# Kernel tuning notes

Hardware: AMD Instinct MI355X
Metric: run time of the kernel (lower is better)

The kernel has to match this reference:

```python
import jax, jax.numpy as jnp
import numpy as np

D_MODEL = 1024
NUM_HEADS = 16
HEAD_DIM = D_MODEL // NUM_HEADS
THETA = 10000.0
B, S = 1, 2048


def setup_inputs() -> dict:
    key = jax.random.key(0)
    ks = jax.random.split(key, 7)
    sc = 0.02
    return {
        "query": jax.random.normal(ks[0], (B, S, D_MODEL), jnp.float32),
        "key": jax.random.normal(ks[1], (B, S, D_MODEL), jnp.float32),
        "value": jax.random.normal(ks[2], (B, S, D_MODEL), jnp.float32),
        "qkv_w": jax.random.normal(ks[3], (3 * D_MODEL, D_MODEL), jnp.float32) * sc,
        "qkv_b": jax.random.normal(ks[4], (3 * D_MODEL,), jnp.float32) * sc,
        "out_w": jax.random.normal(ks[5], (D_MODEL, D_MODEL), jnp.float32) * sc,
        "out_b": jax.random.normal(ks[6], (D_MODEL,), jnp.float32) * sc,
    }


def _rope_cos_sin(seq_len, head_dim, dtype):
    # freqs_for='lang': inv_freq = theta^(-2i/d), i = 0..d/2-1
    inv_freq = 1.0 / (THETA ** (jnp.arange(0, head_dim, 2, dtype=jnp.float32) / head_dim))
    t = jnp.arange(seq_len, dtype=jnp.float32)
    freqs = jnp.outer(t, inv_freq)                      # [S, d/2]
    emb = jnp.concatenate([freqs, freqs], axis=-1)      # [S, d] (non-interleaved)
    return jnp.cos(emb).astype(dtype), jnp.sin(emb).astype(dtype)


def _rotate_half(x):
    half = x.shape[-1] // 2
    return jnp.concatenate([-x[..., half:], x[..., :half]], axis=-1)


def reference(query, key, value, qkv_w, qkv_b, out_w, out_b):
    # NOTE: module computes q,k,v all from `query` (key/value args unused).
    b, s, d = query.shape
    qkv = query @ qkv_w.T + qkv_b                       # [B,S,3D]
    qkv = qkv.reshape(b, s, 3, NUM_HEADS, HEAD_DIM)
    qkv = jnp.transpose(qkv, (2, 0, 3, 1, 4))           # [3,B,H,S,hd]
    q, k, v = qkv[0], qkv[1], qkv[2]

    cos, sin = _rope_cos_sin(s, HEAD_DIM, query.dtype)  # [S,hd]
    q = q * cos + _rotate_half(q) * sin
    k = k * cos + _rotate_half(k) * sin

    scale = 1.0 / np.sqrt(HEAD_DIM)
    scores = jnp.einsum('bhqd,bhkd->bhqk', q, k) * scale
    attn = jax.nn.softmax(scores, axis=-1)
    ctx = jnp.einsum('bhqk,bhkd->bhqd', attn, v)        # [B,H,S,hd]
    ctx = jnp.transpose(ctx, (0, 2, 1, 3)).reshape(b, s, d)
    return ctx @ out_w.T + out_b
```

## Files before the change

kernel.cpp:

```cpp
#include <hip/hip_runtime.h>
#include <math.h>
#include <stdint.h>

#define SEQ 2048
#define DM  1024
#define NH  16
#define HD  64
#define TRI 3072

typedef _Float16 half8 __attribute__((ext_vector_type(8)));
typedef float f32x4 __attribute__((ext_vector_type(4)));

#define GLOAD_LDS16(g, l)                                       \
  __builtin_amdgcn_global_load_lds(                             \
      (__attribute__((address_space(1))) void*)(g),             \
      (__attribute__((address_space(3))) void*)(l), 16, 0, 0)

__global__ __launch_bounds__(256)
void cvt3(const float* __restrict__ s1, const float* __restrict__ s2,
          const float* __restrict__ s3, _Float16* __restrict__ d1,
          _Float16* __restrict__ d2, _Float16* __restrict__ d3,
          float2* __restrict__ tab, int n1, int n2) {
  int b = blockIdx.x;
  if (b >= 6144) {
    int i = (b - 6144) * 256 + threadIdx.x;
    int s = i >> 5, d = i & 31;
    float inv = exp2f((float)d * -0.4152410118609203f);
    float ang = (float)s * inv;
    float sn, cs;
    sincosf(ang, &sn, &cs);
    tab[i] = make_float2(cs, sn);
    return;
  }
  int i = (b * 256 + threadIdx.x) * 4;
  const float* s; _Float16* d;
  if (i < n1)            { s = s1; d = d1; }
  else if (i < n1 + n2)  { s = s2; d = d2; i -= n1; }
  else                   { s = s3; d = d3; i -= n1 + n2; }
  float4 v = *(const float4*)(s + i);
  union { _Float16 h[4]; uint2 u; } pk;
  pk.h[0] = (_Float16)v.x; pk.h[1] = (_Float16)v.y;
  pk.h[2] = (_Float16)v.z; pk.h[3] = (_Float16)v.w;
  *(uint2*)(d + i) = pk.u;
}

template<int ROPE, typename OutT>
__global__ __launch_bounds__(256)
void gemm_dbuf(const _Float16* __restrict__ A, const _Float16* __restrict__ B,
               const float* __restrict__ bias, const float2* __restrict__ tab,
               OutT* __restrict__ C, int M, int N, int K) {
  __shared__ _Float16 As[2][64 * 32];
  __shared__ _Float16 Bs[2][128 * 32];

  const int t = threadIdx.x, lane = t & 63, wv = t >> 6;
  const int l15 = lane & 15, l4 = lane >> 4;
  const int wr = wv >> 1, wc = wv & 1;
  const int bm = blockIdx.y * 64, bn = blockIdx.x * 128;

  auto stage = [&](int buf, int k0) {
    {
      int c = t;
      GLOAD_LDS16(A + (size_t)(bm + (c >> 2)) * K + k0 + (c & 3) * 8,
                  (char*)&As[buf][wv * 512]);
    }
    #pragma unroll
    for (int i = 0; i < 2; ++i) {
      int c = t + i * 256;
      GLOAD_LDS16(B + (size_t)(bn + (c >> 2)) * K + k0 + (c & 3) * 8,
                  (char*)&Bs[buf][(i * 256 + wv * 64) * 8]);
    }
  };

  f32x4 acc[2][4] = {};
  stage(0, 0);
  __syncthreads();

  const int nk = K / 32;
  for (int s = 0; s < nk; ++s) {
    int cur = s & 1;
    if (s + 1 < nk) stage(cur ^ 1, (s + 1) * 32);
    half8 af[2], bf[4];
    #pragma unroll
    for (int mf = 0; mf < 2; ++mf)
      af[mf] = *(const half8*)&As[cur][(wr * 32 + mf * 16 + l15) * 32 + l4 * 8];
    #pragma unroll
    for (int nf = 0; nf < 4; ++nf)
      bf[nf] = *(const half8*)&Bs[cur][(wc * 64 + nf * 16 + l15) * 32 + l4 * 8];
    __builtin_amdgcn_s_setprio(1);
    #pragma unroll
    for (int mf = 0; mf < 2; ++mf)
      #pragma unroll
      for (int nf = 0; nf < 4; ++nf)
        acc[mf][nf] = __builtin_amdgcn_mfma_f32_16x16x32_f16(
            af[mf], bf[nf], acc[mf][nf], 0, 0, 0);
    __builtin_amdgcn_s_setprio(0);
    __syncthreads();
  }

  const int sec = ROPE ? (bn >> 10) : 2;
  float bv[4];
  #pragma unroll
  for (int nf = 0; nf < 4; ++nf) bv[nf] = bias[bn + wc * 64 + nf * 16 + l15];
  #pragma unroll
  for (int mf = 0; mf < 2; ++mf)
    #pragma unroll
    for (int r = 0; r < 4; ++r) {
      int row = bm + wr * 32 + mf * 16 + l4 * 4 + r;
      float v0 = acc[mf][0][r] + bv[0];
      float v1 = acc[mf][1][r] + bv[1];
      float v2 = acc[mf][2][r] + bv[2];
      float v3 = acc[mf][3][r] + bv[3];
      if (ROPE && sec < 2) {
        float2 cs0 = tab[row * 32 + l15];
        float2 cs1 = tab[row * 32 + 16 + l15];
        float a0 = v0 * cs0.x - v2 * cs0.y;
        float a2 = v2 * cs0.x + v0 * cs0.y;
        float a1 = v1 * cs1.x - v3 * cs1.y;
        float a3 = v3 * cs1.x + v1 * cs1.y;
        if (sec == 0) { a0 *= 0.125f; a1 *= 0.125f; a2 *= 0.125f; a3 *= 0.125f; }
        v0 = a0; v1 = a1; v2 = a2; v3 = a3;
      }
      OutT* cr = C + (size_t)row * N + bn + wc * 64 + l15;
      cr[0]  = (OutT)v0; cr[16] = (OutT)v1;
      cr[32] = (OutT)v2; cr[48] = (OutT)v3;
    }
}

__global__ __launch_bounds__(256)
void attn_f16(const _Float16* __restrict__ qkv, _Float16* __restrict__ ctx) {
  __shared__ _Float16 Kl[2][64 * 64];
  __shared__ _Float16 Vt[2][64 * 64];
  __shared__ _Float16 Pl[4][16 * 72];

  const int t = threadIdx.x, lane = t & 63, wv = t >> 6;
  const int l15 = lane & 15, l4 = lane >> 4;
  const int h = blockIdx.y, q0 = blockIdx.x * 64;

  const _Float16* Qb = qkv + h * HD;
  const _Float16* Kb = qkv + DM + h * HD;
  const _Float16* Vb = qkv + 2 * DM + h * HD;

  half8 qf[2];
  {
    const _Float16* qrow = Qb + (size_t)(q0 + wv * 16 + l15) * TRI;
    qf[0] = *(const half8*)(qrow + l4 * 8);
    qf[1] = *(const half8*)(qrow + 32 + l4 * 8);
  }

  uint4 vreg[2];

  auto issueK = [&](int buf, int kt) {
    #pragma unroll
    for (int i = 0; i < 2; ++i) {
      int c = t + i * 256, r = c >> 3, p = c & 7;
      GLOAD_LDS16(Kb + (size_t)(kt + r) * TRI + ((p ^ (r & 7)) * 8),
                  (char*)&Kl[buf][(i * 256 + wv * 64) * 8]);
    }
  };
  auto issueV = [&](int kt) {
    #pragma unroll
    for (int i = 0; i < 2; ++i)
      vreg[i] = *(const uint4*)(Vb + (size_t)(kt + lane) * TRI + (wv + i * 4) * 8);
  };
  auto writeV = [&](int buf) {
    const int m = lane & 3, k0 = lane & 60;
    #pragma unroll
    for (int i = 0; i < 2; ++i) {
      uint32_t u0 = vreg[i].x, u1 = vreg[i].y, u2 = vreg[i].z, u3 = vreg[i].w;
      uint32_t s0 = __shfl_xor(u1, 1), s1 = __shfl_xor(u0, 1);
      uint32_t s2 = __shfl_xor(u3, 1), s3 = __shfl_xor(u2, 1);
      bool b0 = (m & 1);
      uint32_t a0 = b0 ? s0 : u0, a1 = b0 ? u1 : s1;
      uint32_t a2 = b0 ? s2 : u2, a3 = b0 ? u3 : s3;
      uint32_t r0 = __shfl_xor(a2, 2), r1 = __shfl_xor(a3, 2);
      uint32_t r2 = __shfl_xor(a0, 2), r3 = __shfl_xor(a1, 2);
      bool b1 = (m & 2);
      uint32_t w0 = b1 ? r0 : a0, w1 = b1 ? r1 : a1;
      uint32_t w2 = b1 ? a2 : r2, w3 = b1 ? a3 : r3;
      int d0 = (wv + i * 4) * 8 + 2 * m;
      uint32_t lo01 = (w0 & 0xffffu) | (w1 << 16);
      uint32_t lo23 = (w2 & 0xffffu) | (w3 << 16);
      uint32_t hi01 = (w0 >> 16) | (w1 & 0xffff0000u);
      uint32_t hi23 = (w2 >> 16) | (w3 & 0xffff0000u);
      char* base = (char*)Vt[buf];
      int hb = ((k0 >> 2) & 1) * 8;
      *(uint2*)(base + d0 * 128 + (((k0 >> 3) ^ (d0 & 7)) * 16) + hb) =
          make_uint2(lo01, lo23);
      *(uint2*)(base + (d0 + 1) * 128 + (((k0 >> 3) ^ ((d0 + 1) & 7)) * 16) + hb) =
          make_uint2(hi01, hi23);
    }
  };

  float mrun = -3.0e38f, lrun = 0.0f;
  f32x4 o[4] = {};
  _Float16* Pw = Pl[wv];

  issueK(0, 0);
  issueV(0);
  writeV(0);
  __syncthreads();

  const int NT = SEQ / 64;
  for (int tt = 0; tt < NT; ++tt) {
    const int cur = tt & 1;
    const bool pf = (tt + 1 < NT);
    if (pf) { issueK(cur ^ 1, (tt + 1) * 64); issueV((tt + 1) * 64); }

    f32x4 sT[4] = {};
    __builtin_amdgcn_s_setprio(1);
    #pragma unroll
    for (int ds = 0; ds < 2; ++ds)
      #pragma unroll
      for (int mf = 0; mf < 4; ++mf) {
        int r = mf * 16 + l15;
        int cb = ds * 4 + l4;
        half8 kf = *(const half8*)(&Kl[cur][r * 64 + ((cb ^ (r & 7)) * 8)]);
        sT[mf] = __builtin_amdgcn_mfma_f32_16x16x32_f16(kf, qf[ds], sT[mf], 0, 0, 0);
      }
    __builtin_amdgcn_s_setprio(0);

    float mloc = sT[0][0];
    #pragma unroll
    for (int mf = 0; mf < 4; ++mf)
      #pragma unroll
      for (int r = 0; r < 4; ++r) mloc = fmaxf(mloc, sT[mf][r]);
    mloc = fmaxf(mloc, __shfl_xor(mloc, 16));
    mloc = fmaxf(mloc, __shfl_xor(mloc, 32));
    float corr = 1.0f;
    if (!__all(mloc - mrun <= 8.0f)) {
      float mn = fmaxf(mrun, mloc);
      corr = __expf(mrun - mn);
      mrun = mn;
      float cr[4];
      #pragma unroll
      for (int r = 0; r < 4; ++r) cr[r] = __shfl(corr, l4 * 4 + r);
      #pragma unroll
      for (int nf = 0; nf < 4; ++nf)
        #pragma unroll
        for (int r = 0; r < 4; ++r) o[nf][r] *= cr[r];
    }
    float ls = 0.f;
    #pragma unroll
    for (int mf = 0; mf < 4; ++mf)
      #pragma unroll
      for (int r = 0; r < 4; ++r) {
        float p = __expf(sT[mf][r] - mrun);
        sT[mf][r] = p;
        ls += p;
      }
    ls += __shfl_xor(ls, 16);
    ls += __shfl_xor(ls, 32);
    lrun = lrun * corr + ls;

    #pragma unroll
    for (int mf = 0; mf < 4; ++mf) {
      union { _Float16 hh[4]; uint2 u; } pk;
      #pragma unroll
      for (int r = 0; r < 4; ++r) pk.hh[r] = (_Float16)sT[mf][r];
      *(uint2*)(Pw + l15 * 72 + mf * 16 + l4 * 4) = pk.u;
    }

    if (pf) writeV(cur ^ 1);

    __builtin_amdgcn_s_setprio(1);
    #pragma unroll
    for (int ks = 0; ks < 2; ++ks) {
      half8 pa = *(const half8*)(Pw + l15 * 72 + ks * 32 + l4 * 8);
      #pragma unroll
      for (int nf = 0; nf < 4; ++nf) {
        int d = nf * 16 + l15;
        half8 vb = *(const half8*)((char*)Vt[cur] + d * 128 +
                                   (((ks * 4 + l4) ^ (d & 7)) * 16));
        o[nf] = __builtin_amdgcn_mfma_f32_16x16x32_f16(pa, vb, o[nf], 0, 0, 0);
      }
    }
    __builtin_amdgcn_s_setprio(0);
    __syncthreads();
  }

  float lr[4];
  #pragma unroll
  for (int r = 0; r < 4; ++r) lr[r] = 1.0f / __shfl(lrun, l4 * 4 + r);
  #pragma unroll
  for (int nf = 0; nf < 4; ++nf)
    #pragma unroll
    for (int r = 0; r < 4; ++r) {
      int row = q0 + wv * 16 + l4 * 4 + r;
      int col = h * HD + nf * 16 + l15;
      ctx[(size_t)row * DM + col] = (_Float16)(o[nf][r] * lr[r]);
    }
}

extern "C" void kernel_launch(void* const* d_in, const int* in_sizes, int n_in,
                              void* d_out, int out_size, void* d_ws, size_t ws_size,
                              hipStream_t stream) {
  const float* query = (const float*)d_in[0];
  const float* qkv_w = (const float*)d_in[3];
  const float* qkv_b = (const float*)d_in[4];
  const float* out_w = (const float*)d_in[5];
  const float* out_b = (const float*)d_in[6];
  float* out = (float*)d_out;

  _Float16* Aq   = (_Float16*)d_ws;
  _Float16* Wqkv = Aq + (size_t)SEQ * DM;
  _Float16* Wout = Wqkv + (size_t)TRI * DM;
  _Float16* qkv  = Wout + (size_t)DM * DM;
  _Float16* ctx  = qkv + (size_t)SEQ * TRI;
  float2*   tab  = (float2*)(ctx + (size_t)SEQ * DM);

  cvt3<<<6400, 256, 0, stream>>>(query, qkv_w, out_w, Aq, Wqkv, Wout, tab,
                                 SEQ * DM, TRI * DM);

  gemm_dbuf<1, _Float16><<<dim3(TRI / 128, SEQ / 64), 256, 0, stream>>>(
      Aq, Wqkv, qkv_b, tab, qkv, SEQ, TRI, DM);

  attn_f16<<<dim3(SEQ / 64, NH), 256, 0, stream>>>(qkv, ctx);

  gemm_dbuf<0, float><<<dim3(DM / 128, SEQ / 64), 256, 0, stream>>>(
      ctx, Wout, out_b, nullptr, out, SEQ, DM, DM);
}
```

Baseline: 114.6 us.

## Split attention along the key dimension and merge partial softmax results

The attention kernel now runs over two halves of the key sequence as separate blocks in a third grid dimension. Each block writes a partial normalized output plus its running max and sum, and a new merge kernel combines the two halves. This doubles the block count, from 512 to 1024, to fill the GPU's compute units better, at the cost of an extra launch and extra workspace traffic. The P buffer in LDS also moves from padded rows to an XOR-swizzled layout to avoid bank conflicts.

```diff
diff --git a/kernel.cpp b/kernel.cpp
--- a/kernel.cpp
+++ b/kernel.cpp
@@ -7,6 +7,7 @@
 #define NH  16
 #define HD  64
 #define TRI 3072
+#define NSPLIT 2
 
 typedef _Float16 half8 __attribute__((ext_vector_type(8)));
 typedef float f32x4 __attribute__((ext_vector_type(4)));
@@ -127,14 +128,17 @@
 }
 
 __global__ __launch_bounds__(256)
-void attn_f16(const _Float16* __restrict__ qkv, _Float16* __restrict__ ctx) {
+void attn_f16(const _Float16* __restrict__ qkv, _Float16* __restrict__ po,
+              float* __restrict__ pm, float* __restrict__ pl) {
   __shared__ _Float16 Kl[2][64 * 64];
   __shared__ _Float16 Vt[2][64 * 64];
-  __shared__ _Float16 Pl[4][16 * 72];
+  __shared__ _Float16 Pl[4][1024];
 
   const int t = threadIdx.x, lane = t & 63, wv = t >> 6;
   const int l15 = lane & 15, l4 = lane >> 4;
   const int h = blockIdx.y, q0 = blockIdx.x * 64;
+  const int z = blockIdx.z;
+  const int kt0 = z * (SEQ / NSPLIT);
 
   const _Float16* Qb = qkv + h * HD;
   const _Float16* Kb = qkv + DM + h * HD;
@@ -193,18 +197,18 @@
 
   float mrun = -3.0e38f, lrun = 0.0f;
   f32x4 o[4] = {};
-  _Float16* Pw = Pl[wv];
-
-  issueK(0, 0);
-  issueV(0);
+  char* Pw = (char*)Pl[wv];
+
+  issueK(0, kt0);
+  issueV(kt0);
   writeV(0);
   __syncthreads();
 
-  const int NT = SEQ / 64;
+  const int NT = SEQ / NSPLIT / 64;
   for (int tt = 0; tt < NT; ++tt) {
     const int cur = tt & 1;
     const bool pf = (tt + 1 < NT);
-    if (pf) { issueK(cur ^ 1, (tt + 1) * 64); issueV((tt + 1) * 64); }
+    if (pf) { issueK(cur ^ 1, kt0 + (tt + 1) * 64); issueV(kt0 + (tt + 1) * 64); }
 
     f32x4 sT[4] = {};
     __builtin_amdgcn_s_setprio(1);
@@ -257,7 +261,8 @@
       union { _Float16 hh[4]; uint2 u; } pk;
       #pragma unroll
       for (int r = 0; r < 4; ++r) pk.hh[r] = (_Float16)sT[mf][r];
-      *(uint2*)(Pw + l15 * 72 + mf * 16 + l4 * 4) = pk.u;
+      int c = (mf * 2 + (l4 >> 1)) ^ (l15 & 7);
+      *(uint2*)(Pw + l15 * 128 + c * 16 + (l4 & 1) * 8) = pk.u;
     }
 
     if (pf) writeV(cur ^ 1);
@@ -265,7 +270,7 @@
     __builtin_amdgcn_s_setprio(1);
     #pragma unroll
     for (int ks = 0; ks < 2; ++ks) {
-      half8 pa = *(const half8*)(Pw + l15 * 72 + ks * 32 + l4 * 8);
+      half8 pa = *(const half8*)(Pw + l15 * 128 + (((ks * 4 + l4) ^ (l15 & 7)) * 16));
       #pragma unroll
       for (int nf = 0; nf < 4; ++nf) {
         int d = nf * 16 + l15;
@@ -281,14 +286,41 @@
   float lr[4];
   #pragma unroll
   for (int r = 0; r < 4; ++r) lr[r] = 1.0f / __shfl(lrun, l4 * 4 + r);
+  _Float16* pz = po + (size_t)z * SEQ * DM;
   #pragma unroll
   for (int nf = 0; nf < 4; ++nf)
     #pragma unroll
     for (int r = 0; r < 4; ++r) {
       int row = q0 + wv * 16 + l4 * 4 + r;
       int col = h * HD + nf * 16 + l15;
-      ctx[(size_t)row * DM + col] = (_Float16)(o[nf][r] * lr[r]);
-    }
+      pz[(size_t)row * DM + col] = (_Float16)(o[nf][r] * lr[r]);
+    }
+  if (l4 == 0) {
+    int q = q0 + wv * 16 + l15;
+    pm[(z * NH + h) * SEQ + q] = mrun;
+    pl[(z * NH + h) * SEQ + q] = lrun;
+  }
+}
+
+__global__ __launch_bounds__(256)
+void merge2(const _Float16* __restrict__ po, const float* __restrict__ pm,
+            const float* __restrict__ pl, _Float16* __restrict__ ctx) {
+  int e = (blockIdx.x * 256 + threadIdx.x) * 8;
+  int s = e >> 10, h = (e & 1023) >> 6;
+  int idx = h * SEQ + s;
+  float m1 = pm[idx], m2 = pm[NH * SEQ + idx];
+  float l1 = pl[idx], l2 = pl[NH * SEQ + idx];
+  float M = fmaxf(m1, m2);
+  float w1 = __expf(m1 - M) * l1, w2 = __expf(m2 - M) * l2;
+  float inv = 1.0f / (w1 + w2);
+  w1 *= inv; w2 *= inv;
+  half8 a = *(const half8*)(po + e);
+  half8 b = *(const half8*)(po + (size_t)SEQ * DM + e);
+  half8 o;
+  #pragma unroll
+  for (int j = 0; j < 8; ++j)
+    o[j] = (_Float16)(w1 * (float)a[j] + w2 * (float)b[j]);
+  *(half8*)(ctx + e) = o;
 }
 
 extern "C" void kernel_launch(void* const* d_in, const int* in_sizes, int n_in,
@@ -307,6 +339,9 @@
   _Float16* qkv  = Wout + (size_t)DM * DM;
   _Float16* ctx  = qkv + (size_t)SEQ * TRI;
   float2*   tab  = (float2*)(ctx + (size_t)SEQ * DM);
+  _Float16* po = (_Float16*)d_ws;
+  float*    pm = (float*)((char*)d_ws + (8u << 20));
+  float*    pl = pm + NSPLIT * NH * SEQ;
 
   cvt3<<<6400, 256, 0, stream>>>(query, qkv_w, out_w, Aq, Wqkv, Wout, tab,
                                  SEQ * DM, TRI * DM);
@@ -314,7 +349,9 @@
   gemm_dbuf<1, _Float16><<<dim3(TRI / 128, SEQ / 64), 256, 0, stream>>>(
       Aq, Wqkv, qkv_b, tab, qkv, SEQ, TRI, DM);
 
-  attn_f16<<<dim3(SEQ / 64, NH), 256, 0, stream>>>(qkv, ctx);
+  attn_f16<<<dim3(SEQ / 64, NH, NSPLIT), 256, 0, stream>>>(qkv, po, pm, pl);
+
+  merge2<<<SEQ * DM / 8 / 256, 256, 0, stream>>>(po, pm, pl, ctx);
 
   gemm_dbuf<0, float><<<dim3(DM / 128, SEQ / 64), 256, 0, stream>>>(
       ctx, Wout, out_b, nullptr, out, SEQ, DM, DM);
```

After: 120.0 us. 4.7% more time.
